# Kernel optimization log

Measured on AMD Instinct MI355X. Metric: run time of the kernel, lower is better.

The kernel has to match this reference:

```python
import jax, jax.numpy as jnp
import numpy as np

N_AGENTS, BATCH, SDIM, ADIM = 8, 16384, 64, 16
HID, HEADS = 128, 4
ATT_D = HID // HEADS  # 32
EPS = 1e-5


def _bn(x):
    # BatchNorm1d(affine=False), training-mode stats over batch axis (axis=1), biased var
    m = x.mean(axis=1, keepdims=True)
    v = ((x - m) ** 2).mean(axis=1, keepdims=True)
    return (x - m) * jax.lax.rsqrt(v + EPS)


def setup_inputs() -> dict:
    key = jax.random.key(0)
    ks = jax.random.split(key, 16)
    sc = lambda *sh: 1.0 / np.sqrt(sh[-2] if len(sh) > 1 else sh[-1])
    inp = {
        "s": jax.random.normal(ks[0], (N_AGENTS, BATCH, SDIM), jnp.float32),
        "a": jax.random.uniform(ks[1], (N_AGENTS, BATCH, ADIM), jnp.float32),
        # per-agent sa encoder (Attention_Actor): Linear(sdim+adim, hid)
        "W_sa": jax.random.normal(ks[2], (N_AGENTS, SDIM + ADIM, HID), jnp.float32) * (1.0 / np.sqrt(SDIM + ADIM)),
        "b_sa": jnp.zeros((N_AGENTS, HID), jnp.float32),
        # per-agent state encoder: Linear(sdim, hid)
        "W_se": jax.random.normal(ks[3], (N_AGENTS, SDIM, HID), jnp.float32) * (1.0 / np.sqrt(SDIM)),
        "b_se": jnp.zeros((N_AGENTS, HID), jnp.float32),
        # per-head key/selector (no bias) and value (with bias) extractors, shared across agents
        "Wk": jax.random.normal(ks[4], (HEADS, HID, ATT_D), jnp.float32) * (1.0 / np.sqrt(HID)),
        "Wsel": jax.random.normal(ks[5], (HEADS, HID, ATT_D), jnp.float32) * (1.0 / np.sqrt(HID)),
        "Wv": jax.random.normal(ks[6], (HEADS, HID, ATT_D), jnp.float32) * (1.0 / np.sqrt(HID)),
        "bv": jnp.zeros((HEADS, ATT_D), jnp.float32),
        # per-agent critic: Linear(2*hid, hid) -> LeakyReLU -> Linear(hid, adim)
        "Wc1": jax.random.normal(ks[7], (N_AGENTS, 2 * HID, HID), jnp.float32) * (1.0 / np.sqrt(2 * HID)),
        "bc1": jnp.zeros((N_AGENTS, HID), jnp.float32),
        "Wc2": jax.random.normal(ks[8], (N_AGENTS, HID, ADIM), jnp.float32) * (1.0 / np.sqrt(HID)),
        "bc2": jnp.zeros((N_AGENTS, ADIM), jnp.float32),
    }
    return inp


def reference(s, a, W_sa, b_sa, W_se, b_se, Wk, Wsel, Wv, bv, Wc1, bc1, Wc2, bc2):
    lrelu = jax.nn.leaky_relu  # slope 0.01 like nn.LeakyReLU default
    # sa encodings: BN -> Linear -> LeakyReLU, per agent  [N,B,H]
    sa = _bn(jnp.concatenate([s, a], axis=-1))
    e = lrelu(jnp.einsum('nbi,nih->nbh', sa, W_sa) + b_sa[:, None, :])
    # state encodings  [N,B,H]
    se = lrelu(jnp.einsum('nbi,nih->nbh', _bn(s), W_se) + b_se[:, None, :])
    # per-head projections  [P,N,B,D]
    keys = jnp.einsum('nbh,phd->pnbd', e, Wk)
    vals = lrelu(jnp.einsum('nbh,phd->pnbd', e, Wv) + bv[:, None, None, :])
    sel = jnp.einsum('nbh,phd->pnbd', se, Wsel)
    # attention of agent i over agents j != i  [P,N,N,B]
    logits = jnp.einsum('pibd,pjbd->pijb', sel, keys) / np.sqrt(ATT_D).astype(np.float32)
    self_mask = jnp.eye(N_AGENTS, dtype=bool)[None, :, :, None]
    w = jax.nn.softmax(jnp.where(self_mask, -1e9, logits), axis=2)
    other = jnp.einsum('pijb,pjbd->pibd', w, vals)  # [P,N,B,D]
    other_flat = jnp.transpose(other, (1, 2, 0, 3)).reshape(N_AGENTS, BATCH, HEADS * ATT_D)
    # critic: concat(s_enc, head values) -> MLP -> gather Q at argmax action
    critic_in = jnp.concatenate([se, other_flat], axis=-1)  # [N,B,2H]
    h = lrelu(jnp.einsum('nbi,nih->nbh', critic_in, Wc1) + bc1[:, None, :])
    all_q = jnp.einsum('nbh,nho->nbo', h, Wc2) + bc2[:, None, :]  # [N,B,adim]
    int_acs = jnp.argmax(a, axis=-1)[..., None]  # [N,B,1]
    q = jnp.take_along_axis(all_q, int_acs, axis=-1)  # [N,B,1]
    return q
```

## Files before the change

kernel.cpp:

```cpp
#include <hip/hip_runtime.h>


typedef unsigned short u16;
typedef unsigned int u32;

#define NA 8
#define BATCH 16384
#define SD 64
#define AD 16
#define IND 80
#define HID 128
#define HEADS 4
#define ATT 32
#define EPS 1e-5f
#define KP 136
#define KP3 104
#define KPS 72
#define VTS 68
#define WBS 24

using short8 = __attribute__((ext_vector_type(8))) short;
using float4f = __attribute__((ext_vector_type(4))) float;
using uint4v = __attribute__((ext_vector_type(4))) u32;
#define MFMA16(a, b, c) __builtin_amdgcn_mfma_f32_16x16x32_bf16((a), (b), (c), 0, 0, 0)

__device__ __forceinline__ float bf2f(u16 u) { union { u32 i; float f; } v; v.i = ((u32)u) << 16; return v.f; }
__device__ __forceinline__ float lo2f(u32 w) { union { u32 i; float f; } v; v.i = w << 16; return v.f; }
__device__ __forceinline__ float hi2f(u32 w) { union { u32 i; float f; } v; v.i = w & 0xffff0000u; return v.f; }
__device__ __forceinline__ u16 f2bf(float f) {
  union { float f; u32 i; } v; v.f = f;
  u32 x = v.i;
  x += 0x7fffu + ((x >> 16) & 1u);
  return (u16)(x >> 16);
}
__device__ __forceinline__ float lrelu(float x) { return x > 0.f ? x : 0.01f * x; }
__device__ __forceinline__ float ldin(const void* p, size_t i, bool bf) {
  return bf ? bf2f(((const u16*)p)[i]) : ((const float*)p)[i];
}
__device__ __forceinline__ u16 ldbf(const void* p, size_t i, bool bf) {
  return bf ? ((const u16*)p)[i] : f2bf(((const float*)p)[i]);
}
__device__ __forceinline__ short8 lds_s8(const u16* p) {
  union { short8 v; u32 u[4]; } t;
  const u32* q = (const u32*)p;
  t.u[0] = q[0]; t.u[1] = q[1]; t.u[2] = q[2]; t.u[3] = q[3];
  return t.v;
}
__device__ __forceinline__ void barlg() {
  asm volatile("s_waitcnt lgkmcnt(0)" ::: "memory");
  __builtin_amdgcn_s_barrier();
}

__global__ __launch_bounds__(256) void k_prep2(
    const void* __restrict__ s, const void* __restrict__ a,
    const void* __restrict__ Wsa, const void* __restrict__ Wse,
    const void* __restrict__ Wsl, const void* __restrict__ Wk, const void* __restrict__ Wv,
    const void* __restrict__ Wc1,
    int* __restrict__ flag, float* __restrict__ part,
    u16* __restrict__ Wsa_t, u16* __restrict__ Wse_t, u16* __restrict__ Wp_t, u16* __restrict__ Wc1t) {
  __shared__ u16 T[80 * 130];
  __shared__ float S0[256], Q0[256], S1[256], Q1[256];
  __shared__ int cnt[2];
  int tid = threadIdx.x;
  if (tid < 2) cnt[tid] = 0;
  __syncthreads();
  {
    u32 wv = ((const u32*)s)[tid];
    u32 lo = wv & 0xffffu, e = (lo >> 7) & 0xffu;
    if (lo == 0u || lo == 0x8000u) atomicAdd(&cnt[1], 1);
    else if (e < 0x70u || e > 0x8fu) atomicAdd(&cnt[0], 1);
  }
  __syncthreads();
  bool bf = !(cnt[0] >= 64 || cnt[1] >= 192);
  if (blockIdx.x == 0 && tid == 0) *flag = bf ? 1 : 0;
  int blkr = blockIdx.x;
  if (blkr < 2048) {
    int n = blkr >> 8, c = blkr & 255, b0 = c << 6;
    float* p = part + (size_t)(n * 256 + c) * 160;
    {
      int f2 = tid & 31, rg = tid >> 5;
      float s0 = 0.f, s1 = 0.f, q0 = 0.f, q1 = 0.f;
      #pragma unroll
      for (int i = 0; i < 8; i++) {
        int b = b0 + rg + 8 * i;
        float x0, x1;
        if (bf) { u32 wv = ((const u32*)s)[((size_t)n * BATCH + b) * 32 + f2]; x0 = lo2f(wv); x1 = hi2f(wv); }
        else { const float* sf = (const float*)s + ((size_t)n * BATCH + b) * 64 + 2 * f2; x0 = sf[0]; x1 = sf[1]; }
        s0 += x0; q0 += x0 * x0; s1 += x1; q1 += x1 * x1;
      }
      S0[tid] = s0; Q0[tid] = q0; S1[tid] = s1; Q1[tid] = q1;
    }
    __syncthreads();
    if (tid < 64) {
      int f2 = tid >> 1, odd = tid & 1;
      float S = 0.f, Q = 0.f;
      #pragma unroll
      for (int rg = 0; rg < 8; rg++) {
        int ix = rg * 32 + f2;
        S += odd ? S1[ix] : S0[ix];
        Q += odd ? Q1[ix] : Q0[ix];
      }
      p[tid * 2] = S; p[tid * 2 + 1] = Q;
    }
    __syncthreads();
    {
      int f2 = tid & 7, rg = tid >> 3;
      float s0 = 0.f, s1 = 0.f, q0 = 0.f, q1 = 0.f;
      #pragma unroll
      for (int i = 0; i < 2; i++) {
        int b = b0 + rg + 32 * i;
        float x0, x1;
        if (bf) { u32 wv = ((const u32*)a)[((size_t)n * BATCH + b) * 8 + f2]; x0 = lo2f(wv); x1 = hi2f(wv); }
        else { const float* af = (const float*)a + ((size_t)n * BATCH + b) * 16 + 2 * f2; x0 = af[0]; x1 = af[1]; }
        s0 += x0; q0 += x0 * x0; s1 += x1; q1 += x1 * x1;
      }
      S0[tid] = s0; Q0[tid] = q0; S1[tid] = s1; Q1[tid] = q1;
    }
    __syncthreads();
    if (tid < 16) {
      int f2 = tid >> 1, odd = tid & 1;
      float S = 0.f, Q = 0.f;
      #pragma unroll
      for (int rg = 0; rg < 32; rg++) {
        int ix = rg * 8 + f2;
        S += odd ? S1[ix] : S0[ix];
        Q += odd ? Q1[ix] : Q0[ix];
      }
      p[(SD + tid) * 2] = S; p[(SD + tid) * 2 + 1] = Q;
    }
    return;
  }
  int blk = blkr - 2048;
  if (blk < 32) {
    int n = blk >> 2, k0 = (blk & 3) * 64;
    for (int i = tid; i < 64 * 128; i += 256) {
      int kr = i >> 7, cc = i & 127;
      T[kr * 130 + cc] = ldbf(Wc1, ((size_t)n * 256 + k0 + kr) * 128 + cc, bf);
    }
    __syncthreads();
    for (int i = tid; i < 128 * 64; i += 256) {
      int col = i >> 6, kk = i & 63;
      Wc1t[((size_t)n * 128 + col) * 256 + k0 + kk] = T[kk * 130 + col];
    }
  } else if (blk < 40) {
    int n = blk - 32;
    for (int i = tid; i < 80 * 128; i += 256) {
      int kr = i >> 7, cc = i & 127;
      T[kr * 130 + cc] = ldbf(Wsa, ((size_t)n * IND + kr) * 128 + cc, bf);
    }
    __syncthreads();
    for (int i = tid; i < 128 * KP3; i += 256) {
      int col = i / KP3, k = i - col * KP3;
      Wsa_t[((size_t)n * 128 + col) * KP3 + k] = (k < IND) ? T[k * 130 + col] : (u16)0;
    }
  } else if (blk < 48) {
    int n = blk - 40;
    for (int i = tid; i < 64 * 128; i += 256) {
      int kr = i >> 7, cc = i & 127;
      T[kr * 130 + cc] = ldbf(Wse, ((size_t)n * SD + kr) * 128 + cc, bf);
    }
    __syncthreads();
    for (int i = tid; i < 128 * KPS; i += 256) {
      int col = i / KPS, k = i - col * KPS;
      Wse_t[((size_t)n * 128 + col) * KPS + k] = (k < SD) ? T[k * 130 + col] : (u16)0;
    }
  } else {
    int pm = blk - 48, p = pm / 3, mat = pm - 3 * p;
    const void* W = (mat == 0) ? Wsl : (mat == 1) ? Wk : Wv;
    for (int i = tid; i < 128 * 32; i += 256) {
      int kr = i >> 5, d = i & 31;
      T[kr * 34 + d] = ldbf(W, ((size_t)p * HID + kr) * ATT + d, bf);
    }
    __syncthreads();
    for (int i = tid; i < 32 * KP; i += 256) {
      int d = i / KP, k = i - d * KP;
      Wp_t[((size_t)mat * HID + p * ATT + d) * KP + k] = (k < HID) ? T[k * 34 + d] : (u16)0;
    }
  }
}

__global__ __launch_bounds__(256) void k_fin(const float* __restrict__ part, float* __restrict__ mst_g) {
  int n = blockIdx.x;
  int t = threadIdx.x;
  if (t < 160) {
    const float* p = part + (size_t)n * 256 * 160 + t;
    float acc = 0.f;
    #pragma unroll 8
    for (int c = 0; c < 256; c++) acc += p[(size_t)c * 160];
    float other = __shfl_xor(acc, 1);
    if ((t & 1) == 0) {
      float mean = acc * (1.f / BATCH);
      float var = other * (1.f / BATCH) - mean * mean;
      mst_g[(size_t)n * 160 + t] = mean;
      mst_g[(size_t)n * 160 + t + 1] = rsqrtf(var + EPS);
    }
  }
}

__global__ __launch_bounds__(256) void k_enc7(
    const void* __restrict__ s, const void* __restrict__ a,
    const u16* __restrict__ Wsa_t, const void* __restrict__ bsa,
    const u16* __restrict__ Wse_t, const void* __restrict__ bse,
    const u16* __restrict__ Wp_t, const void* __restrict__ bv_g,
    const float* __restrict__ mst_g, const int* __restrict__ flag,
    u16* __restrict__ SEo, u16* __restrict__ SEL2, u16* __restrict__ KEY2, u16* __restrict__ VAL2) {
  __shared__ __align__(16) u16 A[64 * KP];
  __shared__ __align__(16) u16 Bt[64 * KP];
  __shared__ float mst[IND * 2];
  __shared__ float bsaf[HID], bsef[HID], bvf[HID];
  bool bf = (*flag != 0);
  int tid = threadIdx.x;
  int n = blockIdx.y;
  int b0 = blockIdx.x * 64;
  int w = tid >> 6, lane = tid & 63, q = lane >> 4, rl = lane & 15;
  if (tid < HID) {
    bsaf[tid] = ldin(bsa, n * HID + tid, bf);
    bsef[tid] = ldin(bse, n * HID + tid, bf);
    bvf[tid]  = ldin(bv_g, tid, bf);
  }
  if (tid < IND * 2) mst[tid] = mst_g[(size_t)n * IND * 2 + tid];
  barlg();
  for (int i = tid; i < 64 * 32; i += 256) {
    int row = i >> 5, kp = i & 31;
    float x0, x1;
    if (bf) { u32 wv = ((const u32*)s)[((size_t)n * BATCH + b0 + row) * 32 + kp]; x0 = lo2f(wv); x1 = hi2f(wv); }
    else { const float* sf = (const float*)s + ((size_t)n * BATCH + b0 + row) * 64 + 2 * kp; x0 = sf[0]; x1 = sf[1]; }
    int k = 2 * kp;
    u32 o = (u32)f2bf((x0 - mst[k * 2]) * mst[k * 2 + 1]) |
            ((u32)f2bf((x1 - mst[k * 2 + 2]) * mst[k * 2 + 3]) << 16);
    *(u32*)&A[row * KP + k] = o;
  }
  for (int i = tid; i < 64 * 8; i += 256) {
    int row = i >> 3, kp = i & 7;
    float x0, x1;
    if (bf) { u32 wv = ((const u32*)a)[((size_t)n * BATCH + b0 + row) * 8 + kp]; x0 = lo2f(wv); x1 = hi2f(wv); }
    else { const float* af = (const float*)a + ((size_t)n * BATCH + b0 + row) * 16 + 2 * kp; x0 = af[0]; x1 = af[1]; }
    int k = SD + 2 * kp;
    u32 o = (u32)f2bf((x0 - mst[k * 2]) * mst[k * 2 + 1]) |
            ((u32)f2bf((x1 - mst[k * 2 + 2]) * mst[k * 2 + 3]) << 16);
    *(u32*)&A[row * KP + k] = o;
  }
  for (int i = tid; i < 64 * 8; i += 256) {
    int row = i >> 3, c2 = i & 7;
    *(u32*)&A[row * KP + IND + 2 * c2] = 0u;
  }
  barlg();
  const u16* WS = Wse_t + (size_t)n * HID * KPS;
  const u16* WA = Wsa_t + (size_t)n * HID * KP3;
  {
    float4f accS[8] = {};
    #pragma unroll
    for (int kc = 0; kc < 2; kc++) {
      short8 a0 = *(const short8*)&A[(w * 16 + rl) * KP + kc * 32 + q * 8];
      #pragma unroll
      for (int nt = 0; nt < 8; nt++) {
        short8 bb = *(const short8*)(WS + (size_t)(nt * 16 + rl) * KPS + kc * 32 + q * 8);
        accS[nt] = MFMA16(a0, bb, accS[nt]);
      }
    }
    #pragma unroll
    for (int nt = 0; nt < 8; nt++)
      #pragma unroll
      for (int r = 0; r < 4; r++) {
        int row = w * 16 + q * 4 + r, col = nt * 16 + rl;
        u16 v = f2bf(lrelu(accS[nt][r] + bsef[col]));
        SEo[((size_t)n * BATCH + b0 + row) * HID + col] = v;
        Bt[row * KP + col] = v;
      }
  }
  __builtin_amdgcn_sched_barrier(0);
  {
    float4f accE[8] = {};
    #pragma unroll
    for (int kc = 0; kc < 3; kc++) {
      short8 a0 = *(const short8*)&A[(w * 16 + rl) * KP + kc * 32 + q * 8];
      #pragma unroll
      for (int nt = 0; nt < 8; nt++) {
        short8 bb = *(const short8*)(WA + (size_t)(nt * 16 + rl) * KP3 + kc * 32 + q * 8);
        accE[nt] = MFMA16(a0, bb, accE[nt]);
      }
    }
    barlg();
    #pragma unroll
    for (int nt = 0; nt < 8; nt++)
      #pragma unroll
      for (int r = 0; r < 4; r++) {
        int row = w * 16 + q * 4 + r, col = nt * 16 + rl;
        A[row * KP + col] = f2bf(lrelu(accE[nt][r] + bsaf[col]));
      }
  }
  barlg();
  const u16* WSL = Wp_t;
  const u16* WKm = Wp_t + (size_t)HID * KP;
  const u16* WVm = Wp_t + (size_t)2 * HID * KP;
  {
    float4f ac[4][2] = {};
    #pragma unroll
    for (int kc = 0; kc < 4; kc++) {
      short8 af[4];
      #pragma unroll
      for (int mt = 0; mt < 4; mt++)
        af[mt] = *(const short8*)&A[(mt * 16 + rl) * KP + kc * 32 + q * 8];
      #pragma unroll
      for (int nt = 0; nt < 2; nt++) {
        short8 bk = *(const short8*)(WKm + (size_t)(w * 32 + nt * 16 + rl) * KP + kc * 32 + q * 8);
        #pragma unroll
        for (int mt = 0; mt < 4; mt++)
          ac[mt][nt] = MFMA16(af[mt], bk, ac[mt][nt]);
      }
    }
    #pragma unroll
    for (int mt = 0; mt < 4; mt++)
      #pragma unroll
      for (int nt = 0; nt < 2; nt++)
        #pragma unroll
        for (int r = 0; r < 4; r++) {
          int row = mt * 16 + q * 4 + r, col = w * 32 + nt * 16 + rl;
          KEY2[((size_t)(b0 + row) * NA + n) * HID + col] = f2bf(ac[mt][nt][r]);
        }
  }
  __builtin_amdgcn_sched_barrier(0);
  {
    float4f ac[4][2] = {};
    #pragma unroll
    for (int kc = 0; kc < 4; kc++) {
      short8 af[4];
      #pragma unroll
      for (int mt = 0; mt < 4; mt++)
        af[mt] = *(const short8*)&A[(mt * 16 + rl) * KP + kc * 32 + q * 8];
      #pragma unroll
      for (int nt = 0; nt < 2; nt++) {
        short8 bv8 = *(const short8*)(WVm + (size_t)(w * 32 + nt * 16 + rl) * KP + kc * 32 + q * 8);
        #pragma unroll
        for (int mt = 0; mt < 4; mt++)
          ac[mt][nt] = MFMA16(af[mt], bv8, ac[mt][nt]);
      }
    }
    #pragma unroll
    for (int mt = 0; mt < 4; mt++)
      #pragma unroll
      for (int nt = 0; nt < 2; nt++)
        #pragma unroll
        for (int r = 0; r < 4; r++) {
          int row = mt * 16 + q * 4 + r, col = w * 32 + nt * 16 + rl;
          VAL2[((size_t)(b0 + row) * NA + n) * HID + col] = f2bf(lrelu(ac[mt][nt][r] + bvf[col]));
        }
  }
  __builtin_amdgcn_sched_barrier(0);
  {
    float4f ac[4][2] = {};
    #pragma unroll
    for (int kc = 0; kc < 4; kc++) {
      short8 af[4];
      #pragma unroll
      for (int mt = 0; mt < 4; mt++)
        af[mt] = *(const short8*)&Bt[(mt * 16 + rl) * KP + kc * 32 + q * 8];
      #pragma unroll
      for (int nt = 0; nt < 2; nt++) {
        short8 bl = *(const short8*)(WSL + (size_t)(w * 32 + nt * 16 + rl) * KP + kc * 32 + q * 8);
        #pragma unroll
        for (int mt = 0; mt < 4; mt++)
          ac[mt][nt] = MFMA16(af[mt], bl, ac[mt][nt]);
      }
    }
    #pragma unroll
    for (int mt = 0; mt < 4; mt++)
      #pragma unroll
      for (int nt = 0; nt < 2; nt++)
        #pragma unroll
        for (int r = 0; r < 4; r++) {
          int row = mt * 16 + q * 4 + r, col = w * 32 + nt * 16 + rl;
          SEL2[((size_t)(b0 + row) * NA + n) * HID + col] = f2bf(ac[mt][nt][r]);
        }
  }
}

__global__ __launch_bounds__(256) void k_attn2(
    u16* SELO, const u16* __restrict__ KEY, const u16* __restrict__ VAL) {
  __shared__ __align__(16) u16 valt[HEADS * ATT * VTS];
  __shared__ u16 wb[64 * WBS];
  int tid = threadIdx.x;
  size_t r0 = (size_t)blockIdx.x * 64;
  int w = tid >> 6, lane = tid & 63, q = lane >> 4, rl = lane & 15;
  const size_t fbase = (r0 + w * 16 + rl) * HID;
  short8 sa = *(const short8*)(SELO + fbase + q * 8);
  short8 kb = *(const short8*)(KEY + fbase + q * 8);
  {
    const u32* vu = (const u32*)VAL;
    #pragma unroll
    for (int t = 0; t < 16; t++) {
      int idx = tid + t * 256;
      int rp = idx >> 6, c2 = idx & 63;
      u32 wv = vu[(r0 + rp) * 64 + c2];
      int c = 2 * c2;
      valt[c * VTS + rp] = (u16)(wv & 0xffffu);
      valt[(c + 1) * VTS + rp] = (u16)(wv >> 16);
    }
  }
  barlg();
  const float scale = 0.17677669529663687f;
  #pragma unroll
  for (int p = 0; p < HEADS; p++) {
    short8 nsa = sa, nkb = kb;
    if (p < HEADS - 1) {
      nsa = *(const short8*)(SELO + fbase + (p + 1) * ATT + q * 8);
      nkb = *(const short8*)(KEY + fbase + (p + 1) * ATT + q * 8);
    }
    float4f zc = {};
    float4f c = MFMA16(sa, kb, zc);
    int nn = rl;
    #pragma unroll
    for (int r = 0; r < 4; r++) {
      int row = q * 4 + r;
      float x = c[r] * scale;
      if (row == nn) x = -1e9f;
      float mx = x;
      mx = fmaxf(mx, __shfl_xor(mx, 1));
      mx = fmaxf(mx, __shfl_xor(mx, 2));
      mx = fmaxf(mx, __shfl_xor(mx, 4));
      float e = __expf(x - mx);
      float ssum = e;
      ssum += __shfl_xor(ssum, 1);
      ssum += __shfl_xor(ssum, 2);
      ssum += __shfl_xor(ssum, 4);
      float wv = e / ssum;
      if ((row >> 3) != (nn >> 3)) wv = 0.f;
      wb[(w * 16 + row) * WBS + nn] = f2bf(wv);
    }
    short8 aw;
    if (q < 2) aw = *(const short8*)&wb[(w * 16 + rl) * WBS + q * 8];
    else { short8 z = {}; aw = z; }
    float4f o[2] = {};
    #pragma unroll
    for (int nt = 0; nt < 2; nt++) {
      short8 bv8 = lds_s8(&valt[(p * ATT + nt * 16 + rl) * VTS + w * 16 + (q & 1) * 8]);
      o[nt] = MFMA16(aw, bv8, o[nt]);
    }
    #pragma unroll
    for (int nt = 0; nt < 2; nt++)
      #pragma unroll
      for (int r = 0; r < 4; r++) {
        int row = q * 4 + r;
        int rp = w * 16 + (row >> 3) * 8 + (row & 7);
        SELO[(r0 + rp) * HID + p * ATT + nt * 16 + rl] = f2bf(o[nt][r]);
      }
    sa = nsa; kb = nkb;
  }
}

__global__ __launch_bounds__(256) void k_critic2(
    const u16* __restrict__ SEi, const u16* __restrict__ OT, const void* __restrict__ a_g,
    const u16* __restrict__ Wc1t, const void* __restrict__ bc1_g,
    const void* __restrict__ Wc2_g, const void* __restrict__ bc2_g,
    const int* __restrict__ flag, void* __restrict__ qo) {
  __shared__ __align__(16) u16 Xt[128 * KP];
  __shared__ float wc2f[HID * AD];
  __shared__ float bc1f[HID];
  __shared__ int amax[128];
  bool bf = (*flag != 0);
  int tid = threadIdx.x;
  int n = blockIdx.y;
  int b0 = blockIdx.x * 128;
  int w = tid >> 6, lane = tid & 63, q = lane >> 4, rl = lane & 15;
  if (tid < HID) bc1f[tid] = ldin(bc1_g, n * HID + tid, bf);
  {
    int b = tid >> 1, half = tid & 1;
    float best; int bi;
    if (bf) {
      const uint4v* pa = (const uint4v*)((const u32*)a_g + ((size_t)n * BATCH + b0 + b) * 8 + half * 4);
      uint4v x = *pa;
      float v[8] = {lo2f(x[0]), hi2f(x[0]), lo2f(x[1]), hi2f(x[1]),
                    lo2f(x[2]), hi2f(x[2]), lo2f(x[3]), hi2f(x[3])};
      best = v[0]; bi = 0;
      #pragma unroll
      for (int j = 1; j < 8; j++) if (v[j] > best) { best = v[j]; bi = j; }
    } else {
      const float* pa = (const float*)a_g + ((size_t)n * BATCH + b0 + b) * 16 + half * 8;
      float4f v0 = *(const float4f*)pa, v1 = *(const float4f*)(pa + 4);
      float v[8] = {v0[0], v0[1], v0[2], v0[3], v1[0], v1[1], v1[2], v1[3]};
      best = v[0]; bi = 0;
      #pragma unroll
      for (int j = 1; j < 8; j++) if (v[j] > best) { best = v[j]; bi = j; }
    }
    float ob = __shfl_xor(best, 1);
    int obi = __shfl_xor(bi, 1);
    if (half == 0) amax[b] = (ob > best) ? (obi + 8) : bi;
  }
  for (int idx = tid; idx < HID * AD; idx += 256)
    wc2f[idx] = ldin(Wc2_g, (size_t)n * HID * AD + idx, bf);
  const u16* WT = Wc1t + (size_t)n * HID * 256;

  float4f acc[8][2] = {};
  for (int ph = 0; ph < 2; ph++) {
    for (int idx = tid; idx < 128 * 64; idx += 256) {
      int row = idx >> 6, c = idx & 63;
      u32 wv;
      if (ph == 0) wv = ((const u32*)SEi)[((size_t)n * BATCH + b0 + row) * 64 + c];
      else         wv = ((const u32*)OT)[((size_t)(b0 + row) * NA + n) * 64 + c];
      ((u32*)&Xt[row * KP])[c] = wv;
    }
    barlg();
    #pragma unroll
    for (int kc = 0; kc < 4; kc++) {
      int ko = ph * HID + kc * 32;
      short8 bb0 = *(const short8*)(WT + (size_t)(w * 32 + rl) * 256 + ko + q * 8);
      short8 bb1 = *(const short8*)(WT + (size_t)(w * 32 + 16 + rl) * 256 + ko + q * 8);
      #pragma unroll
      for (int mt = 0; mt < 8; mt++) {
        short8 af = *(const short8*)&Xt[(mt * 16 + rl) * KP + kc * 32 + q * 8];
        acc[mt][0] = MFMA16(af, bb0, acc[mt][0]);
        acc[mt][1] = MFMA16(af, bb1, acc[mt][1]);
      }
    }
    barlg();
  }
  u16* ht = Xt;
  #pragma unroll
  for (int mt = 0; mt < 8; mt++)
    #pragma unroll
    for (int nt = 0; nt < 2; nt++)
      #pragma unroll
      for (int r = 0; r < 4; r++) {
        int row = mt * 16 + q * 4 + r, col = w * 32 + nt * 16 + rl;
        ht[row * KP + col] = f2bf(lrelu(acc[mt][nt][r] + bc1f[col]));
      }
  barlg();
  {
    int b = tid >> 1, half = tid & 1;
    int col = amax[b];
    float acq = 0.f;
    const u16* hr = &ht[b * KP + half * 64];
    const float* wz = &wc2f[(half * 64) * AD + col];
    #pragma unroll
    for (int kk = 0; kk < 8; kk++) {
      short8 hv = lds_s8(hr + kk * 8);
      #pragma unroll
      for (int j = 0; j < 8; j++)
        acq = fmaf(bf2f((u16)hv[j]), wz[(kk * 8 + j) * AD], acq);
    }
    acq += __shfl_xor(acq, 1);
    if (half == 0) {
      float v = acq + ldin(bc2_g, n * AD + col, bf);
      size_t oidx = (size_t)n * BATCH + b0 + b;
      if (bf) ((u16*)qo)[oidx] = f2bf(v);
      else    ((float*)qo)[oidx] = v;
    }
  }
}

extern "C" void kernel_launch(void* const* d_in, const int* in_sizes, int n_in,
                              void* d_out, int out_size, void* d_ws, size_t ws_size,
                              hipStream_t stream) {
  const void* s   = d_in[0];
  const void* a   = d_in[1];
  const void* Wsa = d_in[2];
  const void* bsa = d_in[3];
  const void* Wse = d_in[4];
  const void* bse = d_in[5];
  const void* Wk  = d_in[6];
  const void* Wsl = d_in[7];
  const void* Wv  = d_in[8];
  const void* bv  = d_in[9];
  const void* Wc1 = d_in[10];
  const void* bc1 = d_in[11];
  const void* Wc2 = d_in[12];
  const void* bc2 = d_in[13];

  char* ws = (char*)d_ws;
  int*   flag  = (int*)ws;
  float* part  = (float*)(ws + 1024);
  float* mst_g = (float*)(ws + 1311744);
  u16*   Wsa_t = (u16*)(ws + 1316864);
  u16*   Wse_t = (u16*)(ws + 1529856);
  u16*   Wp_t  = (u16*)(ws + 1677312);
  u16*   Wc1t  = (u16*)(ws + 1781760);
  u16*   SEb   = (u16*)(ws + 2306048);
  u16*   SEL   = (u16*)(ws + 2306048 + 1ull * 33554432ull);
  u16*   KEY   = (u16*)(ws + 2306048 + 2ull * 33554432ull);
  u16*   VAL   = (u16*)(ws + 2306048 + 3ull * 33554432ull);

  k_prep2<<<2108, 256, 0, stream>>>(s, a, Wsa, Wse, Wsl, Wk, Wv, Wc1,
                                    flag, part, Wsa_t, Wse_t, Wp_t, Wc1t);
  k_fin<<<NA, 256, 0, stream>>>(part, mst_g);
  k_enc7<<<dim3(BATCH / 64, NA), 256, 0, stream>>>(s, a, Wsa_t, bsa, Wse_t, bse, Wp_t, bv,
                                                   mst_g, flag, SEb, SEL, KEY, VAL);
  k_attn2<<<BATCH / 8, 256, 0, stream>>>(SEL, KEY, VAL);
  k_critic2<<<dim3(BATCH / 128, NA), 256, 0, stream>>>(SEb, SEL, a, Wc1t, bc1, Wc2, bc2, flag, d_out);
}
```

Measured before the change: 247.8 us.

## Fuse encoder and attention kernels into one batch-tiled kernel across all agents

Merges the per-agent encoder kernel and the attention kernel into one 512-thread kernel. Each block handles 16 batch rows for all 8 agents, with one wave per agent. Selector, key and value projections stay in shared memory, so the SEL/KEY/VAL intermediates are never written to or read back from global memory. The cost is more barriers per head, larger shared-memory use, and less reuse of the weight fragments loaded per MFMA. There is also a risk from the hard-coded mapping of wave index to agent with 512 threads.

```diff
diff --git a/kernel.cpp b/kernel.cpp
--- a/kernel.cpp
+++ b/kernel.cpp
@@ -16,7 +16,8 @@
 #define KP 136
 #define KP3 104
 #define KPS 72
-#define VTS 68
+#define SP 34
+#define VTS2 136
 #define WBS 24
 
 using short8 = __attribute__((ext_vector_type(8))) short;
@@ -197,215 +198,153 @@
   }
 }
 
-__global__ __launch_bounds__(256) void k_enc7(
+__global__ __launch_bounds__(512, 4) void k_fused(
     const void* __restrict__ s, const void* __restrict__ a,
     const u16* __restrict__ Wsa_t, const void* __restrict__ bsa,
     const u16* __restrict__ Wse_t, const void* __restrict__ bse,
     const u16* __restrict__ Wp_t, const void* __restrict__ bv_g,
     const float* __restrict__ mst_g, const int* __restrict__ flag,
-    u16* __restrict__ SEo, u16* __restrict__ SEL2, u16* __restrict__ KEY2, u16* __restrict__ VAL2) {
-  __shared__ __align__(16) u16 A[64 * KP];
-  __shared__ __align__(16) u16 Bt[64 * KP];
-  __shared__ float mst[IND * 2];
-  __shared__ float bsaf[HID], bsef[HID], bvf[HID];
+    u16* __restrict__ SEo, u16* __restrict__ OT2) {
+  __shared__ __align__(16) u16 A[128 * KP];
+  __shared__ __align__(16) u16 scr[128 * SP];
+  __shared__ __align__(16) u16 valt[ATT * VTS2];
+  __shared__ u16 wb[128 * WBS];
+  __shared__ float mst[NA * 160];
   bool bf = (*flag != 0);
   int tid = threadIdx.x;
-  int n = blockIdx.y;
-  int b0 = blockIdx.x * 64;
+  int B0 = blockIdx.x * 16;
   int w = tid >> 6, lane = tid & 63, q = lane >> 4, rl = lane & 15;
-  if (tid < HID) {
-    bsaf[tid] = ldin(bsa, n * HID + tid, bf);
-    bsef[tid] = ldin(bse, n * HID + tid, bf);
-    bvf[tid]  = ldin(bv_g, tid, bf);
-  }
-  if (tid < IND * 2) mst[tid] = mst_g[(size_t)n * IND * 2 + tid];
+  for (int i = tid; i < NA * 160; i += 512) mst[i] = mst_g[i];
   barlg();
-  for (int i = tid; i < 64 * 32; i += 256) {
+  for (int i = tid; i < 128 * 32; i += 512) {
     int row = i >> 5, kp = i & 31;
+    int ag = row >> 4, bi = row & 15;
     float x0, x1;
-    if (bf) { u32 wv = ((const u32*)s)[((size_t)n * BATCH + b0 + row) * 32 + kp]; x0 = lo2f(wv); x1 = hi2f(wv); }
-    else { const float* sf = (const float*)s + ((size_t)n * BATCH + b0 + row) * 64 + 2 * kp; x0 = sf[0]; x1 = sf[1]; }
+    if (bf) { u32 wv = ((const u32*)s)[((size_t)ag * BATCH + B0 + bi) * 32 + kp]; x0 = lo2f(wv); x1 = hi2f(wv); }
+    else { const float* sf = (const float*)s + ((size_t)ag * BATCH + B0 + bi) * 64 + 2 * kp; x0 = sf[0]; x1 = sf[1]; }
     int k = 2 * kp;
-    u32 o = (u32)f2bf((x0 - mst[k * 2]) * mst[k * 2 + 1]) |
-            ((u32)f2bf((x1 - mst[k * 2 + 2]) * mst[k * 2 + 3]) << 16);
+    const float* m = &mst[ag * 160];
+    u32 o = (u32)f2bf((x0 - m[k * 2]) * m[k * 2 + 1]) |
+            ((u32)f2bf((x1 - m[k * 2 + 2]) * m[k * 2 + 3]) << 16);
     *(u32*)&A[row * KP + k] = o;
   }
-  for (int i = tid; i < 64 * 8; i += 256) {
+  for (int i = tid; i < 128 * 8; i += 512) {
     int row = i >> 3, kp = i & 7;
+    int ag = row >> 4, bi = row & 15;
     float x0, x1;
-    if (bf) { u32 wv = ((const u32*)a)[((size_t)n * BATCH + b0 + row) * 8 + kp]; x0 = lo2f(wv); x1 = hi2f(wv); }
-    else { const float* af = (const float*)a + ((size_t)n * BATCH + b0 + row) * 16 + 2 * kp; x0 = af[0]; x1 = af[1]; }
+    if (bf) { u32 wv = ((const u32*)a)[((size_t)ag * BATCH + B0 + bi) * 8 + kp]; x0 = lo2f(wv); x1 = hi2f(wv); }
+    else { const float* af = (const float*)a + ((size_t)ag * BATCH + B0 + bi) * 16 + 2 * kp; x0 = af[0]; x1 = af[1]; }
     int k = SD + 2 * kp;
-    u32 o = (u32)f2bf((x0 - mst[k * 2]) * mst[k * 2 + 1]) |
-            ((u32)f2bf((x1 - mst[k * 2 + 2]) * mst[k * 2 + 3]) << 16);
+    const float* m = &mst[ag * 160];
+    u32 o = (u32)f2bf((x0 - m[k * 2]) * m[k * 2 + 1]) |
+            ((u32)f2bf((x1 - m[k * 2 + 2]) * m[k * 2 + 3]) << 16);
     *(u32*)&A[row * KP + k] = o;
   }
-  for (int i = tid; i < 64 * 8; i += 256) {
+  for (int i = tid; i < 128 * 8; i += 512) {
     int row = i >> 3, c2 = i & 7;
     *(u32*)&A[row * KP + IND + 2 * c2] = 0u;
   }
   barlg();
+  const int n = w;
   const u16* WS = Wse_t + (size_t)n * HID * KPS;
   const u16* WA = Wsa_t + (size_t)n * HID * KP3;
-  {
-    float4f accS[8] = {};
-    #pragma unroll
-    for (int kc = 0; kc < 2; kc++) {
-      short8 a0 = *(const short8*)&A[(w * 16 + rl) * KP + kc * 32 + q * 8];
-      #pragma unroll
-      for (int nt = 0; nt < 8; nt++) {
-        short8 bb = *(const short8*)(WS + (size_t)(nt * 16 + rl) * KPS + kc * 32 + q * 8);
-        accS[nt] = MFMA16(a0, bb, accS[nt]);
-      }
-    }
-    #pragma unroll
-    for (int nt = 0; nt < 8; nt++)
-      #pragma unroll
-      for (int r = 0; r < 4; r++) {
-        int row = w * 16 + q * 4 + r, col = nt * 16 + rl;
-        u16 v = f2bf(lrelu(accS[nt][r] + bsef[col]));
-        SEo[((size_t)n * BATCH + b0 + row) * HID + col] = v;
-        Bt[row * KP + col] = v;
-      }
-  }
-  __builtin_amdgcn_sched_barrier(0);
-  {
-    float4f accE[8] = {};
-    #pragma unroll
-    for (int kc = 0; kc < 3; kc++) {
-      short8 a0 = *(const short8*)&A[(w * 16 + rl) * KP + kc * 32 + q * 8];
-      #pragma unroll
-      for (int nt = 0; nt < 8; nt++) {
-        short8 bb = *(const short8*)(WA + (size_t)(nt * 16 + rl) * KP3 + kc * 32 + q * 8);
-        accE[nt] = MFMA16(a0, bb, accE[nt]);
-      }
-    }
-    barlg();
-    #pragma unroll
-    for (int nt = 0; nt < 8; nt++)
-      #pragma unroll
-      for (int r = 0; r < 4; r++) {
-        int row = w * 16 + q * 4 + r, col = nt * 16 + rl;
-        A[row * KP + col] = f2bf(lrelu(accE[nt][r] + bsaf[col]));
-      }
+  float4f accS[8] = {};
+  #pragma unroll
+  for (int kc = 0; kc < 2; kc++) {
+    short8 a0 = *(const short8*)&A[(w * 16 + rl) * KP + kc * 32 + q * 8];
+    #pragma unroll
+    for (int nt = 0; nt < 8; nt++) {
+      short8 bb = *(const short8*)(WS + (size_t)(nt * 16 + rl) * KPS + kc * 32 + q * 8);
+      accS[nt] = MFMA16(a0, bb, accS[nt]);
+    }
+  }
+  float4f accE[8] = {};
+  #pragma unroll
+  for (int kc = 0; kc < 3; kc++) {
+    short8 a0 = *(const short8*)&A[(w * 16 + rl) * KP + kc * 32 + q * 8];
+    #pragma unroll
+    for (int nt = 0; nt < 8; nt++) {
+      short8 bb = *(const short8*)(WA + (size_t)(nt * 16 + rl) * KP3 + kc * 32 + q * 8);
+      accE[nt] = MFMA16(a0, bb, accE[nt]);
+    }
   }
   barlg();
+  #pragma unroll
+  for (int nt = 0; nt < 8; nt++) {
+    int col = nt * 16 + rl;
+    float bias = ldin(bse, n * HID + col, bf);
+    #pragma unroll
+    for (int r = 0; r < 4; r++) {
+      int bi = q * 4 + r;
+      u16 v = f2bf(lrelu(accS[nt][r] + bias));
+      A[(w * 16 + bi) * KP + col] = v;
+      SEo[((size_t)n * BATCH + B0 + bi) * HID + col] = v;
+    }
+  }
   const u16* WSL = Wp_t;
   const u16* WKm = Wp_t + (size_t)HID * KP;
   const u16* WVm = Wp_t + (size_t)2 * HID * KP;
-  {
-    float4f ac[4][2] = {};
+  short8 saf[HEADS];
+  #pragma unroll
+  for (int p = 0; p < HEADS; p++) {
+    float4f ac[2] = {};
     #pragma unroll
     for (int kc = 0; kc < 4; kc++) {
-      short8 af[4];
-      #pragma unroll
-      for (int mt = 0; mt < 4; mt++)
-        af[mt] = *(const short8*)&A[(mt * 16 + rl) * KP + kc * 32 + q * 8];
+      short8 af = *(const short8*)&A[(w * 16 + rl) * KP + kc * 32 + q * 8];
       #pragma unroll
       for (int nt = 0; nt < 2; nt++) {
-        short8 bk = *(const short8*)(WKm + (size_t)(w * 32 + nt * 16 + rl) * KP + kc * 32 + q * 8);
-        #pragma unroll
-        for (int mt = 0; mt < 4; mt++)
-          ac[mt][nt] = MFMA16(af[mt], bk, ac[mt][nt]);
-      }
-    }
-    #pragma unroll
-    for (int mt = 0; mt < 4; mt++)
-      #pragma unroll
-      for (int nt = 0; nt < 2; nt++)
-        #pragma unroll
-        for (int r = 0; r < 4; r++) {
-          int row = mt * 16 + q * 4 + r, col = w * 32 + nt * 16 + rl;
-          KEY2[((size_t)(b0 + row) * NA + n) * HID + col] = f2bf(ac[mt][nt][r]);
-        }
-  }
-  __builtin_amdgcn_sched_barrier(0);
-  {
-    float4f ac[4][2] = {};
+        short8 bl = *(const short8*)(WSL + (size_t)(p * ATT + nt * 16 + rl) * KP + kc * 32 + q * 8);
+        ac[nt] = MFMA16(af, bl, ac[nt]);
+      }
+    }
+    #pragma unroll
+    for (int nt = 0; nt < 2; nt++)
+      #pragma unroll
+      for (int r = 0; r < 4; r++) {
+        int bi = q * 4 + r, d = nt * 16 + rl;
+        scr[(bi * 8 + w) * SP + d] = f2bf(ac[nt][r]);
+      }
+    barlg();
+    saf[p] = lds_s8(&scr[(w * 16 + rl) * SP + q * 8]);
+    barlg();
+  }
+  #pragma unroll
+  for (int nt = 0; nt < 8; nt++) {
+    int col = nt * 16 + rl;
+    float bias = ldin(bsa, n * HID + col, bf);
+    #pragma unroll
+    for (int r = 0; r < 4; r++)
+      A[(w * 16 + q * 4 + r) * KP + col] = f2bf(lrelu(accE[nt][r] + bias));
+  }
+  const float scale = 0.17677669529663687f;
+  #pragma unroll
+  for (int p = 0; p < HEADS; p++) {
+    float4f ak[2] = {}, av[2] = {};
     #pragma unroll
     for (int kc = 0; kc < 4; kc++) {
-      short8 af[4];
-      #pragma unroll
-      for (int mt = 0; mt < 4; mt++)
-        af[mt] = *(const short8*)&A[(mt * 16 + rl) * KP + kc * 32 + q * 8];
+      short8 af = *(const short8*)&A[(w * 16 + rl) * KP + kc * 32 + q * 8];
       #pragma unroll
       for (int nt = 0; nt < 2; nt++) {
-        short8 bv8 = *(const short8*)(WVm + (size_t)(w * 32 + nt * 16 + rl) * KP + kc * 32 + q * 8);
-        #pragma unroll
-        for (int mt = 0; mt < 4; mt++)
-          ac[mt][nt] = MFMA16(af[mt], bv8, ac[mt][nt]);
-      }
-    }
-    #pragma unroll
-    for (int mt = 0; mt < 4; mt++)
-      #pragma unroll
-      for (int nt = 0; nt < 2; nt++)
-        #pragma unroll
-        for (int r = 0; r < 4; r++) {
-          int row = mt * 16 + q * 4 + r, col = w * 32 + nt * 16 + rl;
-          VAL2[((size_t)(b0 + row) * NA + n) * HID + col] = f2bf(lrelu(ac[mt][nt][r] + bvf[col]));
-        }
-  }
-  __builtin_amdgcn_sched_barrier(0);
-  {
-    float4f ac[4][2] = {};
-    #pragma unroll
-    for (int kc = 0; kc < 4; kc++) {
-      short8 af[4];
-      #pragma unroll
-      for (int mt = 0; mt < 4; mt++)
-        af[mt] = *(const short8*)&Bt[(mt * 16 + rl) * KP + kc * 32 + q * 8];
-      #pragma unroll
-      for (int nt = 0; nt < 2; nt++) {
-        short8 bl = *(const short8*)(WSL + (size_t)(w * 32 + nt * 16 + rl) * KP + kc * 32 + q * 8);
-        #pragma unroll
-        for (int mt = 0; mt < 4; mt++)
-          ac[mt][nt] = MFMA16(af[mt], bl, ac[mt][nt]);
-      }
-    }
-    #pragma unroll
-    for (int mt = 0; mt < 4; mt++)
-      #pragma unroll
-      for (int nt = 0; nt < 2; nt++)
-        #pragma unroll
-        for (int r = 0; r < 4; r++) {
-          int row = mt * 16 + q * 4 + r, col = w * 32 + nt * 16 + rl;
-          SEL2[((size_t)(b0 + row) * NA + n) * HID + col] = f2bf(ac[mt][nt][r]);
-        }
-  }
-}
-
-__global__ __launch_bounds__(256) void k_attn2(
-    u16* SELO, const u16* __restrict__ KEY, const u16* __restrict__ VAL) {
-  __shared__ __align__(16) u16 valt[HEADS * ATT * VTS];
-  __shared__ u16 wb[64 * WBS];
-  int tid = threadIdx.x;
-  size_t r0 = (size_t)blockIdx.x * 64;
-  int w = tid >> 6, lane = tid & 63, q = lane >> 4, rl = lane & 15;
-  const size_t fbase = (r0 + w * 16 + rl) * HID;
-  short8 sa = *(const short8*)(SELO + fbase + q * 8);
-  short8 kb = *(const short8*)(KEY + fbase + q * 8);
-  {
-    const u32* vu = (const u32*)VAL;
-    #pragma unroll
-    for (int t = 0; t < 16; t++) {
-      int idx = tid + t * 256;
-      int rp = idx >> 6, c2 = idx & 63;
-      u32 wv = vu[(r0 + rp) * 64 + c2];
-      int c = 2 * c2;
-      valt[c * VTS + rp] = (u16)(wv & 0xffffu);
-      valt[(c + 1) * VTS + rp] = (u16)(wv >> 16);
-    }
-  }
-  barlg();
-  const float scale = 0.17677669529663687f;
-  #pragma unroll
-  for (int p = 0; p < HEADS; p++) {
-    short8 nsa = sa, nkb = kb;
-    if (p < HEADS - 1) {
-      nsa = *(const short8*)(SELO + fbase + (p + 1) * ATT + q * 8);
-      nkb = *(const short8*)(KEY + fbase + (p + 1) * ATT + q * 8);
-    }
+        short8 bk = *(const short8*)(WKm + (size_t)(p * ATT + nt * 16 + rl) * KP + kc * 32 + q * 8);
+        ak[nt] = MFMA16(af, bk, ak[nt]);
+        short8 bv8 = *(const short8*)(WVm + (size_t)(p * ATT + nt * 16 + rl) * KP + kc * 32 + q * 8);
+        av[nt] = MFMA16(af, bv8, av[nt]);
+      }
+    }
+    #pragma unroll
+    for (int nt = 0; nt < 2; nt++) {
+      int d = nt * 16 + rl;
+      float bvv = ldin(bv_g, p * ATT + d, bf);
+      #pragma unroll
+      for (int r = 0; r < 4; r++) {
+        int bi = q * 4 + r, iRow = bi * 8 + w;
+        scr[iRow * SP + d] = f2bf(ak[nt][r]);
+        valt[d * VTS2 + iRow] = f2bf(lrelu(av[nt][r] + bvv));
+      }
+    }
+    barlg();
+    short8 sa = saf[p];
+    short8 kb = lds_s8(&scr[(w * 16 + rl) * SP + q * 8]);
     float4f zc = {};
     float4f c = MFMA16(sa, kb, zc);
     int nn = rl;
@@ -433,7 +372,7 @@
     float4f o[2] = {};
     #pragma unroll
     for (int nt = 0; nt < 2; nt++) {
-      short8 bv8 = lds_s8(&valt[(p * ATT + nt * 16 + rl) * VTS + w * 16 + (q & 1) * 8]);
+      short8 bv8 = lds_s8(&valt[(nt * 16 + rl) * VTS2 + w * 16 + (q & 1) * 8]);
       o[nt] = MFMA16(aw, bv8, o[nt]);
     }
     #pragma unroll
@@ -442,9 +381,9 @@
       for (int r = 0; r < 4; r++) {
         int row = q * 4 + r;
         int rp = w * 16 + (row >> 3) * 8 + (row & 7);
-        SELO[(r0 + rp) * HID + p * ATT + nt * 16 + rl] = f2bf(o[nt][r]);
-      }
-    sa = nsa; kb = nkb;
+        OT2[((size_t)blockIdx.x * 128 + rp) * HID + p * ATT + nt * 16 + rl] = f2bf(o[nt][r]);
+      }
+    barlg();
   }
 }
 
@@ -575,15 +514,12 @@
   u16*   Wp_t  = (u16*)(ws + 1677312);
   u16*   Wc1t  = (u16*)(ws + 1781760);
   u16*   SEb   = (u16*)(ws + 2306048);
-  u16*   SEL   = (u16*)(ws + 2306048 + 1ull * 33554432ull);
-  u16*   KEY   = (u16*)(ws + 2306048 + 2ull * 33554432ull);
-  u16*   VAL   = (u16*)(ws + 2306048 + 3ull * 33554432ull);
+  u16*   OT2   = (u16*)(ws + 2306048 + 1ull * 33554432ull);
 
   k_prep2<<<2108, 256, 0, stream>>>(s, a, Wsa, Wse, Wsl, Wk, Wv, Wc1,
                                     flag, part, Wsa_t, Wse_t, Wp_t, Wc1t);
   k_fin<<<NA, 256, 0, stream>>>(part, mst_g);
-  k_enc7<<<dim3(BATCH / 64, NA), 256, 0, stream>>>(s, a, Wsa_t, bsa, Wse_t, bse, Wp_t, bv,
-                                                   mst_g, flag, SEb, SEL, KEY, VAL);
-  k_attn2<<<BATCH / 8, 256, 0, stream>>>(SEL, KEY, VAL);
-  k_critic2<<<dim3(BATCH / 128, NA), 256, 0, stream>>>(SEb, SEL, a, Wc1t, bc1, Wc2, bc2, flag, d_out);
-}
+  k_fused<<<BATCH / 16, 512, 0, stream>>>(s, a, Wsa_t, bsa, Wse_t, bse, Wp_t, bv,
+                                          mst_g, flag, SEb, OT2);
+  k_critic2<<<dim3(BATCH / 128, NA), 256, 0, stream>>>(SEb, OT2, a, Wc1t, bc1, Wc2, bc2, flag, d_out);
+}
```

Measured after the change: 256.3 us. 3.4% more time.
